# Performance work log

Measured on AMD Instinct MI355X. Metric: run time of the kernel, lower is better.

## Reference

```python
import jax, jax.numpy as jnp
import numpy as np

B, S, D, H, NB = 32, 1024, 512, 16, 12
DH = (D * 3 // H) // 3            # 32: per-head q/k/v dim (Dense outputs 3*DH=96)
V = 8185
FF = 4 * D                        # 2048
EPS = 1e-3                        # keras LayerNormalization default epsilon


def _pos_encoding(seq_len, d_model):
    pos = np.arange(seq_len)[:, None].astype(np.float32)
    i = np.arange(d_model)[None, :].astype(np.float32)
    ang = pos / np.power(10000.0, 2.0 * (i // 2) / np.float32(d_model))
    ang[:, 0::2] = np.sin(ang[:, 0::2])
    ang[:, 1::2] = np.cos(ang[:, 1::2])
    return jnp.asarray(ang[None], jnp.float32)  # [1, S, D]


def _ln(x, g, b):
    m = jnp.mean(x, axis=-1, keepdims=True)
    v = jnp.var(x, axis=-1, keepdims=True)
    return (x - m) * jax.lax.rsqrt(v + EPS) * g + b


def _attn_head(x, W, b, scale):
    # x: [B, S, d_in]; W: [d_in, 3*DH]
    d = x @ W + b
    q, k, v = jnp.split(d, 3, axis=-1)                       # each [B, S, DH]
    # NOTE: original scales by rsqrt(seq_len), not rsqrt(head_dim)
    a = jax.nn.softmax(jnp.einsum('bqd,bkd->bqk', q, k) * scale, axis=-1)
    return jnp.einsum('bqk,bkd->bqd', a, v)                  # [B, S, DH]


def setup_inputs() -> dict:
    key = jax.random.key(0)
    ks = jax.random.split(key, 10)
    def n(k, shape, s=0.02):
        return jax.random.normal(k, shape, jnp.float32) * s
    return dict(
        tokens=jax.random.randint(ks[0], (B, S), 0, V, dtype=jnp.int32),
        emb=n(ks[1], (V, D)),
        # head 0 projection sees D-dim input; heads 1..15 see the previous
        # head's DH-dim output (keras Dense builds lazily -> chained heads)
        W0=n(ks[2], (NB, D, 3 * DH)), b0=jnp.zeros((NB, 3 * DH), jnp.float32),
        Wh=n(ks[3], (NB, H - 1, DH, 3 * DH)), bh=jnp.zeros((NB, H - 1, 3 * DH), jnp.float32),
        Wo=n(ks[4], (NB, D, D)), bo=jnp.zeros((NB, D), jnp.float32),
        g1=jnp.ones((NB, D), jnp.float32), be1=jnp.zeros((NB, D), jnp.float32),
        W1=n(ks[5], (NB, D, FF)), b1=jnp.zeros((NB, FF), jnp.float32),
        W2=n(ks[6], (NB, FF, D)), b2=jnp.zeros((NB, D), jnp.float32),
        g2=jnp.ones((NB, D), jnp.float32), be2=jnp.zeros((NB, D), jnp.float32),
        Wf=n(ks[7], (D, 1)), bf=jnp.zeros((1,), jnp.float32),
    )


def reference(tokens, emb, W0, b0, Wh, bh, Wo, bo, g1, be1, W1, b1, W2, b2, g2, be2, Wf, bf):
    x = emb[tokens] + _pos_encoding(S, D)                    # [B, S, D]
    scale = 1.0 / np.sqrt(np.float32(S))
    for l in range(NB):
        resid = x
        h = _attn_head(x, W0[l], b0[l], scale)               # head 0: D -> DH
        heads = [h]
        for i in range(H - 1):                               # sequentially chained heads
            h = _attn_head(h, Wh[l, i], bh[l, i], scale)     # DH -> DH
            heads.append(h)
        x = jnp.concatenate(heads, axis=-1) @ Wo[l] + bo[l] + resid
        x = _ln(x, g1[l], be1[l])
        r2 = x
        x = jax.nn.relu(x @ W1[l] + b1[l]) @ W2[l] + b2[l] + r2
        x = _ln(x, g2[l], be2[l])
    pooled = jnp.mean(x, axis=1)                             # [B, D]
    logits = pooled @ Wf + bf                                # [B, 1]
    return logits, jax.nn.sigmoid(logits)
```

## Files before the change

### kernel.cpp

```cpp
#include <hip/hip_runtime.h>
#include <math.h>


typedef unsigned short u16;
typedef unsigned int   u32;
typedef __bf16 bf16x8 __attribute__((ext_vector_type(8)));
typedef float  f32x4  __attribute__((ext_vector_type(4)));
typedef u16    u16x8  __attribute__((ext_vector_type(8)));
typedef u16    u16x4  __attribute__((ext_vector_type(4)));

#define SEQ 1024
#define NROWS 32768

#define OFF_W0T 0
#define OFF_WHT 49152
#define OFF_WOT 95232
#define OFF_W1T 357376
#define OFF_W2T 1405952
#define OFF_MQ  2454528
#define WSTRIDE_E 2469888ull

__device__ __forceinline__ float b2f(u16 u) { return __uint_as_float(((u32)u) << 16); }
__device__ __forceinline__ u16 f2b(float f) {
  u32 u = __float_as_uint(f);
  u32 r = (u + 0x7fffu + ((u >> 16) & 1u)) >> 16;
  return (u16)r;
}

#define GLDS16(gp, lp) __builtin_amdgcn_global_load_lds( \
    (__attribute__((address_space(1))) void*)(void*)(gp), \
    (__attribute__((address_space(3))) void*)(void*)(lp), 16, 0, 0)

__global__ __launch_bounds__(256) void gemm128(
    const u16* __restrict__ A, int lda,
    const u16* __restrict__ BT,
    const float* __restrict__ bias,
    const u16* resid,
    u16* C, int ldc,
    int K, int epi)
{
  __shared__ __align__(16) u16 As[128 * 32];
  __shared__ __align__(16) u16 Bs[128 * 32];
  const int tid = threadIdx.x;
  const int lane = tid & 63, wid = tid >> 6;
  const int wm = wid & 1, wn = wid >> 1;
  const int m16 = lane & 15, g4 = lane >> 4;
  const size_t blockM = (size_t)blockIdx.y * 128;
  const size_t blockN = (size_t)blockIdx.x * 128;

  f32x4 acc[4][4] = {};

  for (int k0 = 0; k0 < K; k0 += 32) {
    __syncthreads();
#pragma unroll
    for (int i = 0; i < 2; ++i) {
      int flat = wid * 2048 + i * 1024 + lane * 16;
      int row  = flat >> 6;
      int slot = (flat >> 4) & 3;
      int gch  = slot ^ (row & 3);
      const u16* ga = A + (blockM + row) * (size_t)lda + (size_t)(k0 + gch * 8);
      GLDS16(ga, &As[wid * 1024 + i * 512]);
      const u16* gb = BT + (blockN + row) * (size_t)K + (size_t)(k0 + gch * 8);
      GLDS16(gb, &Bs[wid * 1024 + i * 512]);
    }
    __syncthreads();
    bf16x8 af[4], bfr[4];
#pragma unroll
    for (int tm = 0; tm < 4; ++tm) {
      int r = wm * 64 + tm * 16 + m16;
      af[tm] = *(const bf16x8*)&As[r * 32 + ((g4 ^ (r & 3)) * 8)];
    }
#pragma unroll
    for (int tn = 0; tn < 4; ++tn) {
      int r = wn * 64 + tn * 16 + m16;
      bfr[tn] = *(const bf16x8*)&Bs[r * 32 + ((g4 ^ (r & 3)) * 8)];
    }
#pragma unroll
    for (int tm = 0; tm < 4; ++tm)
#pragma unroll
      for (int tn = 0; tn < 4; ++tn)
        acc[tm][tn] = __builtin_amdgcn_mfma_f32_16x16x32_bf16(bfr[tn], af[tm], acc[tm][tn], 0, 0, 0);
  }

#pragma unroll
  for (int tn = 0; tn < 4; ++tn) {
    size_t colb = blockN + wn * 64 + tn * 16 + g4 * 4;
    f32x4 b4 = {0.f, 0.f, 0.f, 0.f};
    if (epi & 1) b4 = *(const f32x4*)&bias[colb];
#pragma unroll
    for (int tm = 0; tm < 4; ++tm) {
      size_t row = blockM + wm * 64 + tm * 16 + m16;
      size_t off = row * (size_t)ldc + colb;
      f32x4 v = acc[tm][tn];
      if (epi & 4) {
        u16x4 rv = *(const u16x4*)&resid[off];
#pragma unroll
        for (int r = 0; r < 4; ++r) v[r] += b2f(rv[r]);
      }
      u16x4 o;
#pragma unroll
      for (int r = 0; r < 4; ++r) {
        float vv = v[r] + b4[r];
        if (epi & 2) vv = fmaxf(vv, 0.f);
        o[r] = f2b(vv);
      }
      *(u16x4*)&C[off] = o;
    }
  }
}

__global__ __launch_bounds__(256) void gemm_proj(
    const u16* __restrict__ A, int lda,
    const u16* __restrict__ BT,
    const float* __restrict__ bias,
    u16* __restrict__ C,
    int K)
{
  __shared__ __align__(16) u16 As[128 * 32];
  __shared__ __align__(16) u16 Bs[96 * 32];
  const int tid = threadIdx.x;
  const int lane = tid & 63, wid = tid >> 6;
  const int wm = wid & 1, wn = wid >> 1;
  const int m16 = lane & 15, g4 = lane >> 4;
  const size_t blockM = (size_t)blockIdx.x * 128;

  f32x4 acc[4][3] = {};

  for (int k0 = 0; k0 < K; k0 += 32) {
    __syncthreads();
    for (int i = tid; i < 512 + 384; i += 256) {
      if (i < 512) {
        int row = i >> 2, slot = i & 3, gch = slot ^ (row & 3);
        u16x8 v = *(const u16x8*)(A + (blockM + row) * (size_t)lda + (size_t)(k0 + gch * 8));
        *(u16x8*)&As[row * 32 + slot * 8] = v;
      } else {
        int j = i - 512;
        int row = j >> 2, slot = j & 3, gch = slot ^ (row & 3);
        u16x8 v = *(const u16x8*)(BT + row * (size_t)K + (size_t)(k0 + gch * 8));
        *(u16x8*)&Bs[row * 32 + slot * 8] = v;
      }
    }
    __syncthreads();
    bf16x8 af[4], bfr[3];
#pragma unroll
    for (int tm = 0; tm < 4; ++tm) {
      int r = wm * 64 + tm * 16 + m16;
      af[tm] = *(const bf16x8*)&As[r * 32 + ((g4 ^ (r & 3)) * 8)];
    }
#pragma unroll
    for (int tn = 0; tn < 3; ++tn) {
      int r = wn * 48 + tn * 16 + m16;
      bfr[tn] = *(const bf16x8*)&Bs[r * 32 + ((g4 ^ (r & 3)) * 8)];
    }
#pragma unroll
    for (int tm = 0; tm < 4; ++tm)
#pragma unroll
      for (int tn = 0; tn < 3; ++tn)
        acc[tm][tn] = __builtin_amdgcn_mfma_f32_16x16x32_bf16(bfr[tn], af[tm], acc[tm][tn], 0, 0, 0);
  }

#pragma unroll
  for (int tn = 0; tn < 3; ++tn) {
    int colb = wn * 48 + tn * 16 + g4 * 4;
    f32x4 b4 = *(const f32x4*)&bias[colb];
#pragma unroll
    for (int tm = 0; tm < 4; ++tm) {
      size_t row = blockM + wm * 64 + tm * 16 + m16;
      u16x4 o;
#pragma unroll
      for (int r = 0; r < 4; ++r) o[r] = f2b(acc[tm][tn][r] + b4[r]);
      *(u16x4*)&C[row * 96 + colb] = o;
    }
  }
}

__global__ __launch_bounds__(256) void attn_kernel(
    const u16* __restrict__ qkv, u16* __restrict__ outp)
{
  __shared__ __align__(16) u16 Qs[64 * 40];
  __shared__ __align__(16) u16 Ks[2][64 * 40];
  __shared__ __align__(16) u16 VTs[2][32 * 72];
  __shared__ __align__(16) u16 Ps[64 * 72];
  const int tid = threadIdx.x;
  const int lane = tid & 63, wid = tid >> 6;
  const int m16 = lane & 15, g4 = lane >> 4;
  const int b = blockIdx.x >> 4, qt = blockIdx.x & 15;
  const size_t base = (size_t)b * SEQ * 96;
  const int srow = tid >> 2, sc = tid & 3;
  const int perm = ((tid & 3) << 1) | ((tid >> 2) & 1);

  {
    u16x8 v = *(const u16x8*)(qkv + base + (size_t)(qt * 64 + srow) * 96 + sc * 8);
    *(u16x8*)&Qs[srow * 40 + sc * 8] = v;
    const u16* kp = qkv + base + (size_t)srow * 96 + 32 + sc * 8;
    u16x8 kv = *(const u16x8*)kp;
    *(u16x8*)&Ks[0][srow * 40 + sc * 8] = kv;
    u16x8 vv = *(const u16x8*)(kp + 32);
#pragma unroll
    for (int jj = 0; jj < 8; ++jj) {
      int j = jj ^ perm;
      VTs[0][(sc * 8 + j) * 72 + srow] = vv[j];
    }
  }
  __syncthreads();
  const bf16x8 qf = *(const bf16x8*)&Qs[(wid * 16 + m16) * 40 + g4 * 8];

  f32x4 oacc0 = {0.f, 0.f, 0.f, 0.f};
  f32x4 oacc1 = {0.f, 0.f, 0.f, 0.f};
  float lsum = 0.f;

  for (int kt = 0; kt < 16; ++kt) {
    int cur = kt & 1;
    u16x8 kn, vn;
    if (kt < 15) {
      const u16* kp = qkv + base + (size_t)((kt + 1) * 64 + srow) * 96 + 32 + sc * 8;
      kn = *(const u16x8*)kp;
      vn = *(const u16x8*)(kp + 32);
    }
    f32x4 st[4];
#pragma unroll
    for (int ct = 0; ct < 4; ++ct) {
      bf16x8 kf = *(const bf16x8*)&Ks[cur][(ct * 16 + m16) * 40 + g4 * 8];
      f32x4 z = {0.f, 0.f, 0.f, 0.f};
      st[ct] = __builtin_amdgcn_mfma_f32_16x16x32_bf16(kf, qf, z, 0, 0, 0);
    }
#pragma unroll
    for (int ct = 0; ct < 4; ++ct) {
      u16x4 pk;
#pragma unroll
      for (int r = 0; r < 4; ++r) {
        float p = exp2f(st[ct][r] * 0.04508422002778f);
        lsum += p;
        pk[r] = f2b(p);
      }
      *(u16x4*)&Ps[(wid * 16 + m16) * 72 + ct * 16 + g4 * 4] = pk;
    }
#pragma unroll
    for (int ks = 0; ks < 2; ++ks) {
      bf16x8 pf  = *(const bf16x8*)&Ps[(wid * 16 + m16) * 72 + ks * 32 + g4 * 8];
      bf16x8 vf0 = *(const bf16x8*)&VTs[cur][(m16) * 72 + ks * 32 + g4 * 8];
      bf16x8 vf1 = *(const bf16x8*)&VTs[cur][(16 + m16) * 72 + ks * 32 + g4 * 8];
      oacc0 = __builtin_amdgcn_mfma_f32_16x16x32_bf16(vf0, pf, oacc0, 0, 0, 0);
      oacc1 = __builtin_amdgcn_mfma_f32_16x16x32_bf16(vf1, pf, oacc1, 0, 0, 0);
    }
    if (kt < 15) {
      int nb = cur ^ 1;
      *(u16x8*)&Ks[nb][srow * 40 + sc * 8] = kn;
#pragma unroll
      for (int jj = 0; jj < 8; ++jj) {
        int j = jj ^ perm;
        VTs[nb][(sc * 8 + j) * 72 + srow] = vn[j];
      }
    }
    __syncthreads();
  }
  lsum += __shfl_xor(lsum, 16, 64);
  lsum += __shfl_xor(lsum, 32, 64);
  float inv = 1.f / lsum;
  size_t row = (size_t)b * SEQ + qt * 64 + wid * 16 + m16;
  u16x4 o0, o1;
#pragma unroll
  for (int r = 0; r < 4; ++r) {
    o0[r] = f2b(oacc0[r] * inv);
    o1[r] = f2b(oacc1[r] * inv);
  }
  *(u16x4*)&outp[row * 512 + g4 * 4]      = o0;
  *(u16x4*)&outp[row * 512 + 16 + g4 * 4] = o1;
}

__global__ __launch_bounds__(256) void attn_chain(
    const u16* __restrict__ xprev,
    const u16* __restrict__ MqkT,
    const u16* __restrict__ WhT,
    const float* __restrict__ bv,
    u16* __restrict__ outp)
{
  __shared__ __align__(16) u16 Xqs[64 * 40];
  __shared__ __align__(16) u16 Hqs[64 * 40];
  __shared__ __align__(16) u16 Mqs[32 * 40];
  __shared__ __align__(16) u16 Wvs[32 * 40];
  __shared__ __align__(16) u16 Xks[2][64 * 40];
  __shared__ __align__(16) u16 XkTs[2][32 * 72];
  __shared__ __align__(16) u16 Ps[64 * 72];
  const int tid = threadIdx.x;
  const int lane = tid & 63, wid = tid >> 6;
  const int m16 = lane & 15, g4 = lane >> 4;
  const int b = blockIdx.x >> 4, qt = blockIdx.x & 15;
  const size_t rbase = (size_t)b * SEQ;
  const int srow = tid >> 2, sc = tid & 3;
  const int perm = ((tid & 3) << 1) | ((tid >> 2) & 1);

  {
    *(u16x8*)&Xqs[srow * 40 + sc * 8] =
        *(const u16x8*)(xprev + (rbase + qt * 64 + srow) * 512 + sc * 8);
    if (tid < 128) {
      int r2 = tid >> 2, c2 = tid & 3;
      *(u16x8*)&Mqs[r2 * 40 + c2 * 8] = *(const u16x8*)(MqkT + r2 * 32 + c2 * 8);
    } else {
      int t2 = tid - 128, r2 = t2 >> 2, c2 = t2 & 3;
      *(u16x8*)&Wvs[r2 * 40 + c2 * 8] = *(const u16x8*)(WhT + (64 + r2) * 32 + c2 * 8);
    }
    u16x8 xv = *(const u16x8*)(xprev + (rbase + srow) * 512 + sc * 8);
    *(u16x8*)&Xks[0][srow * 40 + sc * 8] = xv;
#pragma unroll
    for (int jj = 0; jj < 8; ++jj) {
      int j = jj ^ perm;
      XkTs[0][(sc * 8 + j) * 72 + srow] = xv[j];
    }
  }
  __syncthreads();

  {
    bf16x8 aq = *(const bf16x8*)&Xqs[(wid * 16 + m16) * 40 + g4 * 8];
#pragma unroll
    for (int h = 0; h < 2; ++h) {
      bf16x8 bm = *(const bf16x8*)&Mqs[(h * 16 + m16) * 40 + g4 * 8];
      f32x4 z = {0.f, 0.f, 0.f, 0.f};
      f32x4 hc = __builtin_amdgcn_mfma_f32_16x16x32_bf16(bm, aq, z, 0, 0, 0);
      u16x4 hw;
#pragma unroll
      for (int r = 0; r < 4; ++r) hw[r] = f2b(hc[r]);
      *(u16x4*)&Hqs[(wid * 16 + m16) * 40 + h * 16 + g4 * 4] = hw;
    }
  }
  const bf16x8 hb = *(const bf16x8*)&Hqs[(wid * 16 + m16) * 40 + g4 * 8];

  f32x4 t0 = {0.f, 0.f, 0.f, 0.f};
  f32x4 t1 = {0.f, 0.f, 0.f, 0.f};
  float lsum = 0.f;

  for (int kt = 0; kt < 16; ++kt) {
    int cur = kt & 1;
    u16x8 xn;
    if (kt < 15)
      xn = *(const u16x8*)(xprev + (rbase + (kt + 1) * 64 + srow) * 512 + sc * 8);

    f32x4 st[4];
#pragma unroll
    for (int ct = 0; ct < 4; ++ct) {
      bf16x8 ak = *(const bf16x8*)&Xks[cur][(ct * 16 + m16) * 40 + g4 * 8];
      f32x4 z = {0.f, 0.f, 0.f, 0.f};
      st[ct] = __builtin_amdgcn_mfma_f32_16x16x32_bf16(ak, hb, z, 0, 0, 0);
    }
#pragma unroll
    for (int ct = 0; ct < 4; ++ct) {
      u16x4 pk;
#pragma unroll
      for (int r = 0; r < 4; ++r) {
        float p = exp2f(st[ct][r] * 0.04508422002778f);
        lsum += p;
        pk[r] = f2b(p);
      }
      *(u16x4*)&Ps[(wid * 16 + m16) * 72 + ct * 16 + g4 * 4] = pk;
    }
#pragma unroll
    for (int ks = 0; ks < 2; ++ks) {
      bf16x8 pf = *(const bf16x8*)&Ps[(wid * 16 + m16) * 72 + ks * 32 + g4 * 8];
      bf16x8 x0 = *(const bf16x8*)&XkTs[cur][(m16) * 72 + ks * 32 + g4 * 8];
      bf16x8 x1 = *(const bf16x8*)&XkTs[cur][(16 + m16) * 72 + ks * 32 + g4 * 8];
      t0 = __builtin_amdgcn_mfma_f32_16x16x32_bf16(x0, pf, t0, 0, 0, 0);
      t1 = __builtin_amdgcn_mfma_f32_16x16x32_bf16(x1, pf, t1, 0, 0, 0);
    }
    if (kt < 15) {
      int nb = cur ^ 1;
      *(u16x8*)&Xks[nb][srow * 40 + sc * 8] = xn;
#pragma unroll
      for (int jj = 0; jj < 8; ++jj) {
        int j = jj ^ perm;
        XkTs[nb][(sc * 8 + j) * 72 + srow] = xn[j];
      }
    }
    __syncthreads();
  }
  lsum += __shfl_xor(lsum, 16, 64);
  lsum += __shfl_xor(lsum, 32, 64);
  float inv = 1.f / lsum;
  u16* Ts = Xqs;
  u16x4 tw0, tw1;
#pragma unroll
  for (int r = 0; r < 4; ++r) {
    tw0[r] = f2b(t0[r] * inv);
    tw1[r] = f2b(t1[r] * inv);
  }
  *(u16x4*)&Ts[(wid * 16 + m16) * 40 + g4 * 4]      = tw0;
  *(u16x4*)&Ts[(wid * 16 + m16) * 40 + 16 + g4 * 4] = tw1;
  bf16x8 ta = *(const bf16x8*)&Ts[(wid * 16 + m16) * 40 + g4 * 8];
  size_t row = rbase + qt * 64 + wid * 16 + m16;
#pragma unroll
  for (int h = 0; h < 2; ++h) {
    bf16x8 wv = *(const bf16x8*)&Wvs[(h * 16 + m16) * 40 + g4 * 8];
    f32x4 z = {0.f, 0.f, 0.f, 0.f};
    f32x4 o = __builtin_amdgcn_mfma_f32_16x16x32_bf16(wv, ta, z, 0, 0, 0);
    f32x4 bv4 = *(const f32x4*)&bv[h * 16 + g4 * 4];
    u16x4 ow;
#pragma unroll
    for (int r = 0; r < 4; ++r) ow[r] = f2b(o[r] + bv4[r]);
    *(u16x4*)&outp[row * 512 + h * 16 + g4 * 4] = ow;
  }
}

__global__ __launch_bounds__(256) void ln_kernel(
    const u16* in, const float* __restrict__ g,
    const float* __restrict__ b, u16* outp)
{
  int row = blockIdx.x * 4 + (threadIdx.x >> 6);
  int lane = threadIdx.x & 63;
  const u16* p = in + (size_t)row * 512 + lane * 8;
  u16x8 v = *(const u16x8*)p;
  float f[8]; float s = 0.f, ss = 0.f;
#pragma unroll
  for (int j = 0; j < 8; ++j) { f[j] = b2f(v[j]); s += f[j]; ss += f[j] * f[j]; }
#pragma unroll
  for (int m = 1; m < 64; m <<= 1) { s += __shfl_xor(s, m, 64); ss += __shfl_xor(ss, m, 64); }
  float mean = s * (1.f / 512.f);
  float var = ss * (1.f / 512.f) - mean * mean;
  float rstd = rsqrtf(var + 1e-3f);
  u16x8 o;
#pragma unroll
  for (int j = 0; j < 8; ++j) {
    float gv = g[lane * 8 + j], bvv = b[lane * 8 + j];
    o[j] = f2b((f[j] - mean) * rstd * gv + bvv);
  }
  *(u16x8*)(outp + (size_t)row * 512 + lane * 8) = o;
}

__global__ void embed_kernel(const int* __restrict__ tokens,
                             const float* __restrict__ emb, u16* __restrict__ x)
{
  int bs = blockIdx.x;
  int d0 = threadIdx.x * 4;
  int tok = tokens[bs];
  int s = bs & (SEQ - 1);
  const float4 e = *(const float4*)(emb + (size_t)tok * 512 + d0);
  const float ev[4] = {e.x, e.y, e.z, e.w};
  u16x4 o;
#pragma unroll
  for (int j = 0; j < 4; ++j) {
    int d = d0 + j;
    float fr = (float)(d & ~1);
    float ang = (float)s * exp2f(fr * (-13.287712379549449f / 512.f));
    float pe = (d & 1) ? cosf(ang) : sinf(ang);
    o[j] = f2b(ev[j] + pe);
  }
  *(u16x4*)&x[(size_t)bs * 512 + d0] = o;
}

__global__ __launch_bounds__(256) void final_kernel(
    const u16* __restrict__ x, const float* __restrict__ Wf,
    const float* __restrict__ bfp, float* __restrict__ outp)
{
  int b = blockIdx.x, tid = threadIdx.x, lane = tid & 63, wid = tid >> 6;
  const u16* base = x + (size_t)b * SEQ * 512 + lane * 8;
  float acc[8] = {};
  for (int s = wid; s < SEQ; s += 4) {
    u16x8 v = *(const u16x8*)(base + (size_t)s * 512);
#pragma unroll
    for (int j = 0; j < 8; ++j) acc[j] += b2f(v[j]);
  }
  float dot = 0.f;
#pragma unroll
  for (int j = 0; j < 8; ++j) dot += acc[j] * Wf[lane * 8 + j];
#pragma unroll
  for (int m = 1; m < 64; m <<= 1) dot += __shfl_xor(dot, m, 64);
  __shared__ float red[4];
  if (lane == 0) red[wid] = dot;
  __syncthreads();
  if (tid == 0) {
    float lg = (red[0] + red[1] + red[2] + red[3]) * (1.f / 1024.f) + bfp[0];
    outp[b] = lg;
    outp[32 + b] = 1.f / (1.f + expf(-lg));
  }
}

__global__ void prep_layer(
    const float* __restrict__ W0, const float* __restrict__ Wh,
    const float* __restrict__ Wo, const float* __restrict__ W1,
    const float* __restrict__ W2,
    u16* __restrict__ wb, size_t dstride, int lsrc0)
{
  const int l = lsrc0 + blockIdx.y;
  const float* W0l = W0 + (size_t)l * 512 * 96;
  const float* Whl = Wh + (size_t)l * 15 * 32 * 96;
  const float* Wol = Wo + (size_t)l * 512 * 512;
  const float* W1l = W1 + (size_t)l * 512 * 2048;
  const float* W2l = W2 + (size_t)l * 2048 * 512;
  u16* dstb = wb + (size_t)blockIdx.y * dstride;

  int bid = blockIdx.x;
  if (bid >= 2397) {
    int h = bid - 2397;
    const float* Whh = Whl + (size_t)h * 32 * 96;
    u16* M = dstb + OFF_MQ + h * 1024;
    int e0 = threadIdx.x * 4;
    for (int e = e0; e < e0 + 4; ++e) {
      int a = e >> 5, bb = e & 31;
      float acc = 0.f;
#pragma unroll 8
      for (int d = 0; d < 32; ++d)
        acc += Whh[a * 96 + 32 + d] * Whh[bb * 96 + d];
      M[e] = f2b(acc);
    }
    return;
  }
  const float* src; u16* dst; int R, C, rt, ct;
  if (bid < 48)        { src = W0l; dst = dstb + OFF_W0T; R = 512;  C = 96;   ct = bid % 3;  rt = bid / 3; }
  else if (bid < 93)   { int i = bid - 48; int h = i / 3;
                         src = Whl + (size_t)h * 32 * 96; dst = dstb + OFF_WHT + (size_t)h * 96 * 32;
                         R = 32; C = 96; ct = i % 3; rt = 0; }
  else if (bid < 349)  { int i = bid - 93;   src = Wol; dst = dstb + OFF_WOT; R = 512;  C = 512;  rt = i >> 4; ct = i & 15; }
  else if (bid < 1373) { int i = bid - 349;  src = W1l; dst = dstb + OFF_W1T; R = 512;  C = 2048; rt = i >> 6; ct = i & 63; }
  else                 { int i = bid - 1373; src = W2l; dst = dstb + OFF_W2T; R = 2048; C = 512;  rt = i >> 4; ct = i & 15; }

  __shared__ u16 tile[32][33];
  int c0 = ct * 32, r0 = rt * 32;
  int tc = threadIdx.x & 31, tr = threadIdx.x >> 5;
#pragma unroll
  for (int k = 0; k < 4; ++k) {
    int rr = tr + k * 8;
    tile[rr][tc] = f2b(src[(size_t)(r0 + rr) * C + c0 + tc]);
  }
  __syncthreads();
#pragma unroll
  for (int k = 0; k < 4; ++k) {
    int rr = tr + k * 8;
    dst[(size_t)(c0 + rr) * R + r0 + tc] = tile[tc][rr];
  }
}

extern "C" void kernel_launch(void* const* d_in, const int* in_sizes, int n_in,
                              void* d_out, int out_size, void* d_ws, size_t ws_size,
                              hipStream_t stream) {
  (void)in_sizes; (void)n_in; (void)out_size;
  const int*   tokens = (const int*)d_in[0];
  const float* emb = (const float*)d_in[1];
  const float* W0  = (const float*)d_in[2];
  const float* b0  = (const float*)d_in[3];
  const float* Wh  = (const float*)d_in[4];
  const float* bh  = (const float*)d_in[5];
  const float* Wo  = (const float*)d_in[6];
  const float* bo  = (const float*)d_in[7];
  const float* g1  = (const float*)d_in[8];
  const float* be1 = (const float*)d_in[9];
  const float* W1  = (const float*)d_in[10];
  const float* b1  = (const float*)d_in[11];
  const float* W2  = (const float*)d_in[12];
  const float* b2  = (const float*)d_in[13];
  const float* g2  = (const float*)d_in[14];
  const float* be2 = (const float*)d_in[15];
  const float* Wf  = (const float*)d_in[16];
  const float* bfp = (const float*)d_in[17];
  float* out = (float*)d_out;

  char* w = (char*)d_ws;
  auto carve = [&](size_t bytes) {
    char* p = w; w += (bytes + 255) & ~(size_t)255; return (u16*)p;
  };
  const size_t XB = (size_t)NROWS * 512 * 2;
  const size_t QB = (size_t)NROWS * 96 * 2;
  const size_t WSB = WSTRIDE_E * 2;
  const size_t TF = (size_t)NROWS * 2048 * 2;
  const size_t TH = TF / 2;
  const size_t MGN = 1u << 20;
  const size_t base3 = XB + XB + QB;

  bool allw; int tmode;
  if      (ws_size >= base3 + 12 * WSB + TF + MGN) { allw = true;  tmode = 2; }
  else if (ws_size >= base3 + 12 * WSB + TH + MGN) { allw = true;  tmode = 1; }
  else if (ws_size >= base3 + 1 * WSB + TH + MGN)  { allw = false; tmode = 1; }
  else if (ws_size >= base3 + 12 * WSB + MGN)      { allw = true;  tmode = 0; }
  else                                             { allw = false; tmode = 0; }

  u16* x    = carve(XB);
  u16* xcat = carve(XB);
  u16* qkv  = carve(QB);
  u16* wb   = carve((allw ? 12 : 1) * WSB);
  u16* t    = (tmode == 2) ? carve(TF) : (tmode == 1) ? carve(TH) : xcat;

  embed_kernel<<<NROWS, 128, 0, stream>>>(tokens, emb, x);
  if (allw)
    prep_layer<<<dim3(2412, 12), 256, 0, stream>>>(W0, Wh, Wo, W1, W2,
                                                   wb, WSTRIDE_E, 0);

  for (int l = 0; l < 12; ++l) {
    u16* wbl = wb + (allw ? (size_t)l * WSTRIDE_E : 0);
    if (!allw)
      prep_layer<<<dim3(2412, 1), 256, 0, stream>>>(W0, Wh, Wo, W1, W2,
                                                    wbl, 0, l);
    gemm_proj<<<256, 256, 0, stream>>>(x, 512, wbl + OFF_W0T, b0 + l * 96, qkv, 512);
    attn_kernel<<<512, 256, 0, stream>>>(qkv, xcat);
    for (int i = 0; i < 15; ++i) {
      attn_chain<<<512, 256, 0, stream>>>(
          xcat + i * 32, wbl + OFF_MQ + i * 1024, wbl + OFF_WHT + (size_t)i * 96 * 32,
          bh + (size_t)(l * 15 + i) * 96 + 64, xcat + (i + 1) * 32);
    }
    gemm128<<<dim3(4, 256), 256, 0, stream>>>(xcat, 512, wbl + OFF_WOT, bo + l * 512,
                                              x, x, 512, 512, 1 | 4);
    ln_kernel<<<8192, 256, 0, stream>>>(x, g1 + l * 512, be1 + l * 512, x);
    if (tmode == 2) {
      gemm128<<<dim3(16, 256), 256, 0, stream>>>(x, 512, wbl + OFF_W1T, b1 + l * 2048,
                                                 nullptr, t, 2048, 512, 1 | 2);
      gemm128<<<dim3(4, 256), 256, 0, stream>>>(t, 2048, wbl + OFF_W2T, b2 + l * 512,
                                                x, x, 512, 2048, 1 | 4);
    } else {
      const int nch = (tmode == 1) ? 2 : 4;
      const int rows = NROWS / nch;
      for (int c = 0; c < nch; ++c) {
        const u16* xc = x + (size_t)c * rows * 512;
        gemm128<<<dim3(16, rows / 128), 256, 0, stream>>>(xc, 512, wbl + OFF_W1T,
                                                          b1 + l * 2048, nullptr, t,
                                                          2048, 512, 1 | 2);
        gemm128<<<dim3(4, rows / 128), 256, 0, stream>>>(t, 2048, wbl + OFF_W2T,
                                                         b2 + l * 512, xc, (u16*)xc,
                                                         512, 2048, 1 | 4);
      }
    }
    ln_kernel<<<8192, 256, 0, stream>>>(x, g2 + l * 512, be2 + l * 512, x);
  }

  final_kernel<<<32, 256, 0, stream>>>(x, Wf, bfp, out);
}
```

Before: 9.571 ms.

## Apply V projection per key tile in attn_chain and add 64-row W2 GEMM

The chained-head attention kernel now projects each key tile through the V weights before the PV product, instead of applying Wv to the attention-weighted X at the end. It reads key rows straight from global memory rather than staging X and its transpose in shared memory, which cuts LDS traffic and the transposing scatter stores. The cost is extra MFMA work per tile and a sync placed before the scores. Separately, the FF2 GEMM (K=2048, N=512) switches to a new 64-row tile kernel, doubling the block count so the GPU fills better.

After: 10.19 ms. +6.4%, slower.

```diff
diff --git a/kernel.cpp b/kernel.cpp
--- a/kernel.cpp
+++ b/kernel.cpp
@@ -96,6 +96,90 @@
         u16x4 rv = *(const u16x4*)&resid[off];
 #pragma unroll
         for (int r = 0; r < 4; ++r) v[r] += b2f(rv[r]);
+      }
+      u16x4 o;
+#pragma unroll
+      for (int r = 0; r < 4; ++r) {
+        float vv = v[r] + b4[r];
+        if (epi & 2) vv = fmaxf(vv, 0.f);
+        o[r] = f2b(vv);
+      }
+      *(u16x4*)&C[off] = o;
+    }
+  }
+}
+
+__global__ __launch_bounds__(256) void gemm64(
+    const u16* __restrict__ A, int lda,
+    const u16* __restrict__ BT,
+    const float* __restrict__ bias,
+    const u16* resid,
+    u16* C, int ldc,
+    int K, int epi)
+{
+  __shared__ __align__(16) u16 As[64 * 32];
+  __shared__ __align__(16) u16 Bs[128 * 32];
+  const int tid = threadIdx.x;
+  const int lane = tid & 63, wid = tid >> 6;
+  const int wm = wid & 1, wn = wid >> 1;
+  const int m16 = lane & 15, g4 = lane >> 4;
+  const size_t blockM = (size_t)blockIdx.y * 64;
+  const size_t blockN = (size_t)blockIdx.x * 128;
+
+  f32x4 acc[2][4] = {};
+
+  for (int k0 = 0; k0 < K; k0 += 32) {
+    __syncthreads();
+    {
+      int flat = wid * 1024 + lane * 16;
+      int row  = flat >> 6;
+      int slot = (flat >> 4) & 3;
+      int gch  = slot ^ (row & 3);
+      const u16* ga = A + (blockM + row) * (size_t)lda + (size_t)(k0 + gch * 8);
+      GLDS16(ga, &As[wid * 512]);
+    }
+#pragma unroll
+    for (int i = 0; i < 2; ++i) {
+      int flat = wid * 2048 + i * 1024 + lane * 16;
+      int row  = flat >> 6;
+      int slot = (flat >> 4) & 3;
+      int gch  = slot ^ (row & 3);
+      const u16* gb = BT + (blockN + row) * (size_t)K + (size_t)(k0 + gch * 8);
+      GLDS16(gb, &Bs[wid * 1024 + i * 512]);
+    }
+    __syncthreads();
+    bf16x8 af[2], bfr[4];
+#pragma unroll
+    for (int tm = 0; tm < 2; ++tm) {
+      int r = wm * 32 + tm * 16 + m16;
+      af[tm] = *(const bf16x8*)&As[r * 32 + ((g4 ^ (r & 3)) * 8)];
+    }
+#pragma unroll
+    for (int tn = 0; tn < 4; ++tn) {
+      int r = wn * 64 + tn * 16 + m16;
+      bfr[tn] = *(const bf16x8*)&Bs[r * 32 + ((g4 ^ (r & 3)) * 8)];
+    }
+#pragma unroll
+    for (int tm = 0; tm < 2; ++tm)
+#pragma unroll
+      for (int tn = 0; tn < 4; ++tn)
+        acc[tm][tn] = __builtin_amdgcn_mfma_f32_16x16x32_bf16(bfr[tn], af[tm], acc[tm][tn], 0, 0, 0);
+  }
+
+#pragma unroll
+  for (int tn = 0; tn < 4; ++tn) {
+    size_t colb = blockN + wn * 64 + tn * 16 + g4 * 4;
+    f32x4 b4 = {0.f, 0.f, 0.f, 0.f};
+    if (epi & 1) b4 = *(const f32x4*)&bias[colb];
+#pragma unroll
+    for (int tm = 0; tm < 2; ++tm) {
+      size_t row = blockM + wm * 32 + tm * 16 + m16;
+      size_t off = row * (size_t)ldc + colb;
+      f32x4 v = acc[tm][tn];
+      if (epi & 4) {
+        u16x4 rv = *(const u16x4*)&resid[off];
+#pragma unroll
+      for (int r = 0; r < 4; ++r) v[r] += b2f(rv[r]);
       }
       u16x4 o;
 #pragma unroll
@@ -275,72 +359,58 @@
     const float* __restrict__ bv,
     u16* __restrict__ outp)
 {
-  __shared__ __align__(16) u16 Xqs[64 * 40];
   __shared__ __align__(16) u16 Hqs[64 * 40];
-  __shared__ __align__(16) u16 Mqs[32 * 40];
-  __shared__ __align__(16) u16 Wvs[32 * 40];
-  __shared__ __align__(16) u16 Xks[2][64 * 40];
-  __shared__ __align__(16) u16 XkTs[2][32 * 72];
+  __shared__ __align__(16) u16 VTs[2][32 * 72];
   __shared__ __align__(16) u16 Ps[64 * 72];
   const int tid = threadIdx.x;
   const int lane = tid & 63, wid = tid >> 6;
   const int m16 = lane & 15, g4 = lane >> 4;
   const int b = blockIdx.x >> 4, qt = blockIdx.x & 15;
   const size_t rbase = (size_t)b * SEQ;
-  const int srow = tid >> 2, sc = tid & 3;
-  const int perm = ((tid & 3) << 1) | ((tid >> 2) & 1);
+
+  const bf16x8 wvB0 = *(const bf16x8*)&WhT[(64 + m16) * 32 + g4 * 8];
+  const bf16x8 wvB1 = *(const bf16x8*)&WhT[(64 + 16 + m16) * 32 + g4 * 8];
+  const bf16x8 mqA0 = *(const bf16x8*)&MqkT[(m16) * 32 + g4 * 8];
+  const bf16x8 mqA1 = *(const bf16x8*)&MqkT[(16 + m16) * 32 + g4 * 8];
+  const bf16x8 xqB  = *(const bf16x8*)(xprev + (rbase + qt * 64 + wid * 16 + m16) * 512 + g4 * 8);
 
   {
-    *(u16x8*)&Xqs[srow * 40 + sc * 8] =
-        *(const u16x8*)(xprev + (rbase + qt * 64 + srow) * 512 + sc * 8);
-    if (tid < 128) {
-      int r2 = tid >> 2, c2 = tid & 3;
-      *(u16x8*)&Mqs[r2 * 40 + c2 * 8] = *(const u16x8*)(MqkT + r2 * 32 + c2 * 8);
-    } else {
-      int t2 = tid - 128, r2 = t2 >> 2, c2 = t2 & 3;
-      *(u16x8*)&Wvs[r2 * 40 + c2 * 8] = *(const u16x8*)(WhT + (64 + r2) * 32 + c2 * 8);
-    }
-    u16x8 xv = *(const u16x8*)(xprev + (rbase + srow) * 512 + sc * 8);
-    *(u16x8*)&Xks[0][srow * 40 + sc * 8] = xv;
-#pragma unroll
-    for (int jj = 0; jj < 8; ++jj) {
-      int j = jj ^ perm;
-      XkTs[0][(sc * 8 + j) * 72 + srow] = xv[j];
-    }
-  }
-  __syncthreads();
-
-  {
-    bf16x8 aq = *(const bf16x8*)&Xqs[(wid * 16 + m16) * 40 + g4 * 8];
-#pragma unroll
-    for (int h = 0; h < 2; ++h) {
-      bf16x8 bm = *(const bf16x8*)&Mqs[(h * 16 + m16) * 40 + g4 * 8];
+    f32x4 z = {0.f, 0.f, 0.f, 0.f};
+    f32x4 h0 = __builtin_amdgcn_mfma_f32_16x16x32_bf16(mqA0, xqB, z, 0, 0, 0);
+    f32x4 h1 = __builtin_amdgcn_mfma_f32_16x16x32_bf16(mqA1, xqB, z, 0, 0, 0);
+    u16x4 w0, w1;
+#pragma unroll
+    for (int r = 0; r < 4; ++r) { w0[r] = f2b(h0[r]); w1[r] = f2b(h1[r]); }
+    *(u16x4*)&Hqs[(wid * 16 + m16) * 40 + g4 * 4]      = w0;
+    *(u16x4*)&Hqs[(wid * 16 + m16) * 40 + 16 + g4 * 4] = w1;
+  }
+  const bf16x8 hb = *(const bf16x8*)&Hqs[(wid * 16 + m16) * 40 + g4 * 8];
+
+  f32x4 oacc0 = {0.f, 0.f, 0.f, 0.f};
+  f32x4 oacc1 = {0.f, 0.f, 0.f, 0.f};
+  float lsum = 0.f;
+
+  for (int kt = 0; kt < 16; ++kt) {
+    const int cur = kt & 1;
+    const u16* kb = xprev + (rbase + kt * 64) * 512;
+    {
+      bf16x8 xkw = *(const bf16x8*)(kb + (size_t)(wid * 16 + m16) * 512 + g4 * 8);
       f32x4 z = {0.f, 0.f, 0.f, 0.f};
-      f32x4 hc = __builtin_amdgcn_mfma_f32_16x16x32_bf16(bm, aq, z, 0, 0, 0);
-      u16x4 hw;
-#pragma unroll
-      for (int r = 0; r < 4; ++r) hw[r] = f2b(hc[r]);
-      *(u16x4*)&Hqs[(wid * 16 + m16) * 40 + h * 16 + g4 * 4] = hw;
-    }
-  }
-  const bf16x8 hb = *(const bf16x8*)&Hqs[(wid * 16 + m16) * 40 + g4 * 8];
-
-  f32x4 t0 = {0.f, 0.f, 0.f, 0.f};
-  f32x4 t1 = {0.f, 0.f, 0.f, 0.f};
-  float lsum = 0.f;
-
-  for (int kt = 0; kt < 16; ++kt) {
-    int cur = kt & 1;
-    u16x8 xn;
-    if (kt < 15)
-      xn = *(const u16x8*)(xprev + (rbase + (kt + 1) * 64 + srow) * 512 + sc * 8);
-
+      f32x4 v0 = __builtin_amdgcn_mfma_f32_16x16x32_bf16(xkw, wvB0, z, 0, 0, 0);
+      f32x4 v1 = __builtin_amdgcn_mfma_f32_16x16x32_bf16(xkw, wvB1, z, 0, 0, 0);
+      u16x4 a0, a1;
+#pragma unroll
+      for (int r = 0; r < 4; ++r) { a0[r] = f2b(v0[r]); a1[r] = f2b(v1[r]); }
+      *(u16x4*)&VTs[cur][(m16) * 72 + wid * 16 + g4 * 4]      = a0;
+      *(u16x4*)&VTs[cur][(16 + m16) * 72 + wid * 16 + g4 * 4] = a1;
+    }
+    __syncthreads();
     f32x4 st[4];
 #pragma unroll
     for (int ct = 0; ct < 4; ++ct) {
-      bf16x8 ak = *(const bf16x8*)&Xks[cur][(ct * 16 + m16) * 40 + g4 * 8];
+      bf16x8 xk = *(const bf16x8*)(kb + (size_t)(ct * 16 + m16) * 512 + g4 * 8);
       f32x4 z = {0.f, 0.f, 0.f, 0.f};
-      st[ct] = __builtin_amdgcn_mfma_f32_16x16x32_bf16(ak, hb, z, 0, 0, 0);
+      st[ct] = __builtin_amdgcn_mfma_f32_16x16x32_bf16(xk, hb, z, 0, 0, 0);
     }
 #pragma unroll
     for (int ct = 0; ct < 4; ++ct) {
@@ -355,48 +425,27 @@
     }
 #pragma unroll
     for (int ks = 0; ks < 2; ++ks) {
-      bf16x8 pf = *(const bf16x8*)&Ps[(wid * 16 + m16) * 72 + ks * 32 + g4 * 8];
-      bf16x8 x0 = *(const bf16x8*)&XkTs[cur][(m16) * 72 + ks * 32 + g4 * 8];
-      bf16x8 x1 = *(const bf16x8*)&XkTs[cur][(16 + m16) * 72 + ks * 32 + g4 * 8];
-      t0 = __builtin_amdgcn_mfma_f32_16x16x32_bf16(x0, pf, t0, 0, 0, 0);
-      t1 = __builtin_amdgcn_mfma_f32_16x16x32_bf16(x1, pf, t1, 0, 0, 0);
-    }
-    if (kt < 15) {
-      int nb = cur ^ 1;
-      *(u16x8*)&Xks[nb][srow * 40 + sc * 8] = xn;
-#pragma unroll
-      for (int jj = 0; jj < 8; ++jj) {
-        int j = jj ^ perm;
-        XkTs[nb][(sc * 8 + j) * 72 + srow] = xn[j];
-      }
-    }
-    __syncthreads();
+      bf16x8 pf  = *(const bf16x8*)&Ps[(wid * 16 + m16) * 72 + ks * 32 + g4 * 8];
+      bf16x8 vA0 = *(const bf16x8*)&VTs[cur][(m16) * 72 + ks * 32 + g4 * 8];
+      bf16x8 vA1 = *(const bf16x8*)&VTs[cur][(16 + m16) * 72 + ks * 32 + g4 * 8];
+      oacc0 = __builtin_amdgcn_mfma_f32_16x16x32_bf16(vA0, pf, oacc0, 0, 0, 0);
+      oacc1 = __builtin_amdgcn_mfma_f32_16x16x32_bf16(vA1, pf, oacc1, 0, 0, 0);
+    }
   }
   lsum += __shfl_xor(lsum, 16, 64);
   lsum += __shfl_xor(lsum, 32, 64);
   float inv = 1.f / lsum;
-  u16* Ts = Xqs;
-  u16x4 tw0, tw1;
+  size_t row = rbase + qt * 64 + wid * 16 + m16;
+  f32x4 bv0 = *(const f32x4*)&bv[g4 * 4];
+  f32x4 bv1 = *(const f32x4*)&bv[16 + g4 * 4];
+  u16x4 o0, o1;
 #pragma unroll
   for (int r = 0; r < 4; ++r) {
-    tw0[r] = f2b(t0[r] * inv);
-    tw1[r] = f2b(t1[r] * inv);
-  }
-  *(u16x4*)&Ts[(wid * 16 + m16) * 40 + g4 * 4]      = tw0;
-  *(u16x4*)&Ts[(wid * 16 + m16) * 40 + 16 + g4 * 4] = tw1;
-  bf16x8 ta = *(const bf16x8*)&Ts[(wid * 16 + m16) * 40 + g4 * 8];
-  size_t row = rbase + qt * 64 + wid * 16 + m16;
-#pragma unroll
-  for (int h = 0; h < 2; ++h) {
-    bf16x8 wv = *(const bf16x8*)&Wvs[(h * 16 + m16) * 40 + g4 * 8];
-    f32x4 z = {0.f, 0.f, 0.f, 0.f};
-    f32x4 o = __builtin_amdgcn_mfma_f32_16x16x32_bf16(wv, ta, z, 0, 0, 0);
-    f32x4 bv4 = *(const f32x4*)&bv[h * 16 + g4 * 4];
-    u16x4 ow;
-#pragma unroll
-    for (int r = 0; r < 4; ++r) ow[r] = f2b(o[r] + bv4[r]);
-    *(u16x4*)&outp[row * 512 + h * 16 + g4 * 4] = ow;
-  }
+    o0[r] = f2b(oacc0[r] * inv + bv0[r]);
+    o1[r] = f2b(oacc1[r] * inv + bv1[r]);
+  }
+  *(u16x4*)&outp[row * 512 + g4 * 4]      = o0;
+  *(u16x4*)&outp[row * 512 + 16 + g4 * 4] = o1;
 }
 
 __global__ __launch_bounds__(256) void ln_kernel(
@@ -599,8 +648,8 @@
     if (tmode == 2) {
       gemm128<<<dim3(16, 256), 256, 0, stream>>>(x, 512, wbl + OFF_W1T, b1 + l * 2048,
                                                  nullptr, t, 2048, 512, 1 | 2);
-      gemm128<<<dim3(4, 256), 256, 0, stream>>>(t, 2048, wbl + OFF_W2T, b2 + l * 512,
-                                                x, x, 512, 2048, 1 | 4);
+      gemm64<<<dim3(4, 512), 256, 0, stream>>>(t, 2048, wbl + OFF_W2T, b2 + l * 512,
+                                               x, x, 512, 2048, 1 | 4);
     } else {
       const int nch = (tmode == 1) ? 2 : 4;
       const int rows = NROWS / nch;
@@ -609,9 +658,9 @@
         gemm128<<<dim3(16, rows / 128), 256, 0, stream>>>(xc, 512, wbl + OFF_W1T,
                                                           b1 + l * 2048, nullptr, t,
                                                           2048, 512, 1 | 2);
-        gemm128<<<dim3(4, rows / 128), 256, 0, stream>>>(t, 2048, wbl + OFF_W2T,
-                                                         b2 + l * 512, xc, (u16*)xc,
-                                                         512, 2048, 1 | 4);
+        gemm64<<<dim3(4, rows / 64), 256, 0, stream>>>(t, 2048, wbl + OFF_W2T,
+                                                       b2 + l * 512, xc, (u16*)xc,
+                                                       512, 2048, 1 | 4);
       }
     }
     ln_kernel<<<8192, 256, 0, stream>>>(x, g2 + l * 512, be2 + l * 512, x);
```
